# Performance work log

Hardware: AMD Instinct MI355X
Metric: run time of the kernel (lower is better)

## Reference

```python
import jax, jax.numpy as jnp
import numpy as np

T_STEPS = 32      # discrete samples along each pixel's voting ray
RAY_STEP = 4.0    # pixel stride between ray samples


def setup_inputs() -> dict:
    key = jax.random.key(0)
    k1, k2, k3, k4 = jax.random.split(key, 4)
    B, C, H, W = 2, 22, 480, 640
    label = jax.random.randint(k1, (B, H, W), 0, C, dtype=jnp.int32)
    vertex = jax.random.normal(k2, (B, 3 * C, H, W), dtype=jnp.float32)
    # per-class 3D extents in meters (~0..0.3 m objects)
    extents = jax.random.uniform(k3, (C, 3), dtype=jnp.float32) * 0.3
    # flattened intrinsics [fx, 0, cx, 0, fy, cy, 0, 0, 1]
    intr = jnp.array([572.4, 0.0, 325.3, 0.0, 573.6, 242.0, 0.0, 0.0, 1.0], dtype=jnp.float32)
    meta_data = jnp.tile(intr[None, :], (B, 1))
    gt = jax.random.normal(k4, (B, C, 4, 4), dtype=jnp.float32)
    return {"label": label, "vertex": vertex, "extents": extents,
            "meta_data": meta_data, "gt": gt, "is_train": 0}


def reference(label, vertex, extents, meta_data, gt, is_train):
    B, C3, H, W = vertex.shape
    C = C3 // 3
    HW = H * W
    f32 = jnp.float32

    # Gather each pixel's class-specific vertex prediction: (nx, ny, z)
    v = vertex.reshape(B, C, 3, HW)                        # (B,C,3,HW)
    lab = label.reshape(B, HW)                             # (B,HW) int
    idx = jnp.broadcast_to(lab[:, None, None, :], (B, 1, 3, HW))
    g = jnp.take_along_axis(v, idx, axis=1)[:, 0]          # (B,3,HW)
    nx, ny, z = g[:, 0], g[:, 1], g[:, 2]
    inv_norm = 1.0 / (jnp.sqrt(nx * nx + ny * ny) + 1e-8)
    nx = nx * inv_norm
    ny = ny * inv_norm

    # Pixel coordinates
    pix = jnp.arange(HW, dtype=jnp.int32)
    xs = (pix % W).astype(f32)
    ys = (pix // W).astype(f32)

    # Cast T_STEPS votes along the predicted ray toward the object center
    t = (jnp.arange(1, T_STEPS + 1, dtype=f32) * RAY_STEP)  # (T,)
    px = jnp.round(xs[None, :, None] + nx[:, :, None] * t[None, None, :]).astype(jnp.int32)
    py = jnp.round(ys[None, :, None] + ny[:, :, None] * t[None, None, :]).astype(jnp.int32)
    inb = (px >= 0) & (px < W) & (py >= 0) & (py < H)
    fg = (lab > 0)[:, :, None]                              # background casts no votes
    w = (inb & fg).astype(f32)                              # (B,HW,T)
    flat = jnp.clip(py, 0, H - 1) * W + jnp.clip(px, 0, W - 1)

    # Scatter-accumulate votes into per-class Hough space (B,C,HW)
    b_idx = jnp.arange(B)[:, None, None]
    acc = jnp.zeros((B, C, HW), dtype=f32).at[b_idx, lab[:, :, None], flat].add(w)

    # Peak detection: argmax per (batch, class)
    peak = jnp.argmax(acc, axis=-1)                         # (B,C)
    votes = jnp.max(acc, axis=-1)                           # (B,C)
    cx = (peak % W).astype(f32)
    cy = (peak // W).astype(f32)

    # Mean predicted depth per class (masked mean over that class's pixels)
    b2 = jnp.arange(B)[:, None]
    cnt = jnp.zeros((B, C), dtype=f32).at[b2, lab].add(1.0)
    zsum = jnp.zeros((B, C), dtype=f32).at[b2, lab].add(z)
    depth = zsum / jnp.maximum(cnt, 1.0)

    # Project object extents to image-plane box size: half = 0.5*|extent|*fx/depth
    fx = meta_data[:, 0][:, None]                           # (B,1)
    diag = jnp.linalg.norm(extents, axis=-1)[None, :]       # (1,C)
    half = 0.5 * diag * fx / jnp.maximum(jnp.abs(depth), 1e-3)

    cls = jnp.broadcast_to(jnp.arange(C, dtype=f32)[None, :], (B, C))
    out = jnp.stack([cls, votes,
                     cx - half, cy - half, cx + half, cy + half,
                     cx, cy, depth], axis=-1)               # (B,C,9)
    return out
```

## Files before the change

### kernel.cpp

```cpp
#include <hip/hip_runtime.h>


#define MAXC 32
#define NSEG 4

__global__ __launch_bounds__(512) void emit_kernel(
    const int* __restrict__ label, const float* __restrict__ vertex,
    unsigned short* __restrict__ bucketData, unsigned* __restrict__ cursor,
    unsigned* __restrict__ cnt, float* __restrict__ zsum,
    int C, int H, int W, int HW, int SEGCAP, int NB)
{
    __shared__ unsigned s_bin[512];
    __shared__ unsigned s_rel[512];
    __shared__ unsigned s_gb[512];
    __shared__ unsigned s_ccnt[MAXC];
    __shared__ float s_cz[MAXC];

    int tid = threadIdx.x;
    int b = blockIdx.y;
    int p = blockIdx.x * 512 + tid;
    int seg = blockIdx.x & (NSEG - 1);

    s_bin[tid] = 0u;
    s_rel[tid] = 0u;
    if (tid < MAXC) { s_ccnt[tid] = 0u; s_cz[tid] = 0.0f; }
    __syncthreads();

    int lab = 0;
    unsigned vote[32];
    bool fg = false;
    if (p < HW) {
        lab = label[(size_t)b * HW + p];
        const float* vb = vertex + ((size_t)(b * 3 * C + 3 * lab)) * HW + p;
        float nx = vb[0];
        float ny = vb[(size_t)HW];
        float z  = vb[2 * (size_t)HW];
        atomicAdd(&s_ccnt[lab], 1u);
        atomicAdd(&s_cz[lab], z);
        if (lab > 0) {
            fg = true;
            float nrm = __fsqrt_rn(__fadd_rn(__fmul_rn(nx, nx), __fmul_rn(ny, ny)));
            float inv = __fdiv_rn(1.0f, __fadd_rn(nrm, 1e-8f));
            float nxn = __fmul_rn(nx, inv);
            float nyn = __fmul_rn(ny, inv);
            float xs = (float)(p % W);
            float ys = (float)(p / W);
            #pragma unroll
            for (int i = 1; i <= 32; ++i) {
                float t = (float)i * 4.0f;
                int px = (int)rintf(__fadd_rn(xs, __fmul_rn(nxn, t)));
                int py = (int)rintf(__fadd_rn(ys, __fmul_rn(nyn, t)));
                vote[i - 1] = (px >= 0 && px < W && py >= 0 && py < H)
                            ? ((unsigned)(py << 10) | (unsigned)px) : 0xFFFFFFFFu;
            }
        }
    }
    if (!fg) {
        #pragma unroll
        for (int i = 0; i < 32; ++i) vote[i] = 0xFFFFFFFFu;
    }

    #pragma unroll
    for (int i = 0; i < 32; ++i)
        if (vote[i] != 0xFFFFFFFFu) atomicAdd(&s_bin[vote[i] >> 10], 1u);
    __syncthreads();

    if (tid < H) {
        unsigned n = s_bin[tid];
        s_gb[tid] = n ? atomicAdd(&cursor[seg * NB + b * H + tid], n) : 0u;
    }
    __syncthreads();

    unsigned labsh = (unsigned)lab << 10;
    #pragma unroll
    for (int i = 0; i < 32; ++i) {
        unsigned vt = vote[i];
        if (vt != 0xFFFFFFFFu) {
            unsigned py = vt >> 10;
            unsigned rel = atomicAdd(&s_rel[py], 1u);
            unsigned g = s_gb[py] + rel;
            if (g < (unsigned)SEGCAP)
                bucketData[((size_t)(b * H + py) * NSEG + seg) * SEGCAP + g] =
                    (unsigned short)(labsh | (vt & 1023u));
        }
    }

    if (tid < C) {
        unsigned c = s_ccnt[tid];
        if (c) {
            atomicAdd(&cnt[b * C + tid], c);
            atomicAdd(&zsum[b * C + tid], s_cz[tid]);
        }
    }
}

__global__ __launch_bounds__(256) void hist_kernel(
    const unsigned short* __restrict__ bucketData,
    const unsigned* __restrict__ cursor,
    unsigned long long* __restrict__ keys,
    int C, int H, int W, int SEGCAP, int NB)
{
    extern __shared__ char sm[];
    unsigned* hist = (unsigned*)sm;
    unsigned long long* s_wb =
        (unsigned long long*)(sm + (size_t)(C * W / 2) * 4);

    int tid = threadIdx.x;
    int lane = tid & 63, wave = tid >> 6;
    int py = blockIdx.x;
    int b = blockIdx.y;
    int words = C * W / 2;

    for (int i = tid; i < words; i += 256) hist[i] = 0u;
    __syncthreads();

    int bucket = b * H + py;
    #pragma unroll
    for (int seg = 0; seg < NSEG; ++seg) {
        unsigned n = cursor[seg * NB + bucket];
        if (n > (unsigned)SEGCAP) n = (unsigned)SEGCAP;
        const unsigned short* src =
            bucketData + ((size_t)bucket * NSEG + seg) * SEGCAP;
        for (unsigned i = tid; i < n; i += 256) {
            unsigned r = src[i];
            unsigned idx = (r >> 10) * (unsigned)W + (r & 1023u);
            atomicAdd(&hist[idx >> 1], 1u << ((idx & 1u) * 16));
        }
    }
    __syncthreads();

    unsigned rowbase = (unsigned)py * (unsigned)W;
    for (int c = 0; c < C; ++c) {
        unsigned long long best = 0;
        for (int px = tid; px < W; px += 256) {
            unsigned cv = (hist[(unsigned)(c * W + px) >> 1] >> ((px & 1) * 16)) & 0xFFFFu;
            unsigned long long k = ((unsigned long long)cv << 32)
                                 | (unsigned long long)(0xFFFFFFFFu - (rowbase + px));
            if (k > best) best = k;
        }
        #pragma unroll
        for (int off = 32; off > 0; off >>= 1) {
            unsigned long long o = __shfl_xor(best, off, 64);
            if (o > best) best = o;
        }
        if (lane == 0) s_wb[c * 4 + wave] = best;
    }
    __syncthreads();
    if (tid < C) {
        unsigned long long m = s_wb[tid * 4];
        #pragma unroll
        for (int w2 = 1; w2 < 4; ++w2)
            if (s_wb[tid * 4 + w2] > m) m = s_wb[tid * 4 + w2];
        atomicMax(&keys[b * C + tid], m);
    }
}

__global__ void finalize_kernel(const unsigned long long* __restrict__ keys,
                                const unsigned* __restrict__ cnt,
                                const float* __restrict__ zsum,
                                const float* __restrict__ extents,
                                const float* __restrict__ meta,
                                float* __restrict__ out,
                                int B, int C, int W)
{
    int i = threadIdx.x;
    if (i >= B * C) return;
    int b = i / C, c = i % C;
    unsigned long long k = keys[i];
    unsigned votes = (unsigned)(k >> 32);
    unsigned peak = 0xFFFFFFFFu - (unsigned)(k & 0xFFFFFFFFull);
    float cx = (float)(peak % (unsigned)W);
    float cy = (float)(peak / (unsigned)W);
    float n = (float)cnt[i];
    float depth = zsum[i] / fmaxf(n, 1.0f);
    float fx = meta[b * 9 + 0];
    const float* e = extents + c * 3;
    float diag = sqrtf(e[0] * e[0] + e[1] * e[1] + e[2] * e[2]);
    float half = 0.5f * diag * fx / fmaxf(fabsf(depth), 0.001f);
    float* o = out + (size_t)i * 9;
    o[0] = (float)c;
    o[1] = (float)votes;
    o[2] = cx - half;
    o[3] = cy - half;
    o[4] = cx + half;
    o[5] = cy + half;
    o[6] = cx;
    o[7] = cy;
    o[8] = depth;
}

extern "C" void kernel_launch(void* const* d_in, const int* in_sizes, int n_in,
                              void* d_out, int out_size, void* d_ws, size_t ws_size,
                              hipStream_t stream)
{
    const int* label    = (const int*)d_in[0];
    const float* vertex = (const float*)d_in[1];
    const float* extents= (const float*)d_in[2];
    const float* meta   = (const float*)d_in[3];

    int C = in_sizes[2] / 3;
    int B = in_sizes[3] / 9;
    int HW = in_sizes[0] / B;
    const int W = 640;
    int H = HW / W;
    int NB = B * H;

    size_t keysOff = 0;
    size_t curOff  = keysOff + (size_t)B * C * 8;
    size_t cntOff  = curOff + (size_t)NSEG * NB * 4;
    size_t zsumOff = cntOff + (size_t)B * C * 4;
    size_t zeroEnd = zsumOff + (size_t)B * C * 4;
    size_t dataOff = (zeroEnd + 63) & ~(size_t)63;

    size_t availRec = (ws_size > dataOff) ? (ws_size - dataOff) / ((size_t)NB * NSEG * 2) : 0;
    int SEGCAP = (int)(availRec > 8192 ? 8192 : availRec);
    SEGCAP &= ~63;

    unsigned long long* keys = (unsigned long long*)((char*)d_ws + keysOff);
    unsigned* cursor         = (unsigned*)((char*)d_ws + curOff);
    unsigned* cnt            = (unsigned*)((char*)d_ws + cntOff);
    float* zsum              = (float*)((char*)d_ws + zsumOff);
    unsigned short* bucketData = (unsigned short*)((char*)d_ws + dataOff);

    hipMemsetAsync(d_ws, 0, zeroEnd, stream);

    dim3 egrid((HW + 511) / 512, B);
    emit_kernel<<<egrid, 512, 0, stream>>>(label, vertex, bucketData, cursor,
                                           cnt, zsum, C, H, W, HW, SEGCAP, NB);

    dim3 hgrid(H, B);
    size_t hsm = (size_t)(C * W / 2) * 4 + (size_t)C * 4 * 8;
    hist_kernel<<<hgrid, 256, hsm, stream>>>(bucketData, cursor, keys, C, H, W, SEGCAP, NB);

    finalize_kernel<<<1, 64, 0, stream>>>(keys, cnt, zsum, extents, meta,
                                          (float*)d_out, B, C, W);
}
```

Measured before the change: 121.7 us.

## Split emit kernel into count and scatter passes that recompute ray votes

Splits the single emit kernel into two launches. The first computes ray samples and builds per-block row counts, then reserves global bucket space and stores the per-block offsets in a workspace table. The second recomputes the same ray samples and scatters records using those offsets. This removes the 32-entry per-thread vote array held across barriers, aiming to cut register pressure and raise occupancy. In exchange the label and vertex data are read twice, the ray arithmetic is done twice, and there is an extra launch plus a global offset table.

```diff
diff --git a/kernel.cpp b/kernel.cpp
--- a/kernel.cpp
+++ b/kernel.cpp
@@ -4,15 +4,37 @@
 #define MAXC 32
 #define NSEG 4
 
-__global__ __launch_bounds__(512) void emit_kernel(
+__device__ __forceinline__ void ray_setup(
     const int* __restrict__ label, const float* __restrict__ vertex,
-    unsigned short* __restrict__ bucketData, unsigned* __restrict__ cursor,
+    int C, int HW, int W, int b, int p,
+    int& lab, float& z, bool& fg,
+    float& nxn, float& nyn, float& xs, float& ys)
+{
+    lab = label[(size_t)b * HW + p];
+    const float* vb = vertex + ((size_t)(b * 3 * C + 3 * lab)) * HW + p;
+    float nx = vb[0];
+    float ny = vb[(size_t)HW];
+    z = vb[2 * (size_t)HW];
+    fg = false;
+    nxn = 0.f; nyn = 0.f; xs = 0.f; ys = 0.f;
+    if (lab > 0) {
+        fg = true;
+        float nrm = __fsqrt_rn(__fadd_rn(__fmul_rn(nx, nx), __fmul_rn(ny, ny)));
+        float inv = __fdiv_rn(1.0f, __fadd_rn(nrm, 1e-8f));
+        nxn = __fmul_rn(nx, inv);
+        nyn = __fmul_rn(ny, inv);
+        xs = (float)(p % W);
+        ys = (float)(p / W);
+    }
+}
+
+__global__ __launch_bounds__(512) void emitA_kernel(
+    const int* __restrict__ label, const float* __restrict__ vertex,
+    unsigned* __restrict__ cursor, unsigned* __restrict__ gbTable,
     unsigned* __restrict__ cnt, float* __restrict__ zsum,
-    int C, int H, int W, int HW, int SEGCAP, int NB)
+    int C, int H, int W, int HW, int NB)
 {
     __shared__ unsigned s_bin[512];
-    __shared__ unsigned s_rel[512];
-    __shared__ unsigned s_gb[512];
     __shared__ unsigned s_ccnt[MAXC];
     __shared__ float s_cz[MAXC];
 
@@ -22,67 +44,31 @@
     int seg = blockIdx.x & (NSEG - 1);
 
     s_bin[tid] = 0u;
-    s_rel[tid] = 0u;
     if (tid < MAXC) { s_ccnt[tid] = 0u; s_cz[tid] = 0.0f; }
     __syncthreads();
 
-    int lab = 0;
-    unsigned vote[32];
-    bool fg = false;
     if (p < HW) {
-        lab = label[(size_t)b * HW + p];
-        const float* vb = vertex + ((size_t)(b * 3 * C + 3 * lab)) * HW + p;
-        float nx = vb[0];
-        float ny = vb[(size_t)HW];
-        float z  = vb[2 * (size_t)HW];
+        int lab; float z; bool fg; float nxn, nyn, xs, ys;
+        ray_setup(label, vertex, C, HW, W, b, p, lab, z, fg, nxn, nyn, xs, ys);
         atomicAdd(&s_ccnt[lab], 1u);
         atomicAdd(&s_cz[lab], z);
-        if (lab > 0) {
-            fg = true;
-            float nrm = __fsqrt_rn(__fadd_rn(__fmul_rn(nx, nx), __fmul_rn(ny, ny)));
-            float inv = __fdiv_rn(1.0f, __fadd_rn(nrm, 1e-8f));
-            float nxn = __fmul_rn(nx, inv);
-            float nyn = __fmul_rn(ny, inv);
-            float xs = (float)(p % W);
-            float ys = (float)(p / W);
+        if (fg) {
             #pragma unroll
             for (int i = 1; i <= 32; ++i) {
                 float t = (float)i * 4.0f;
                 int px = (int)rintf(__fadd_rn(xs, __fmul_rn(nxn, t)));
                 int py = (int)rintf(__fadd_rn(ys, __fmul_rn(nyn, t)));
-                vote[i - 1] = (px >= 0 && px < W && py >= 0 && py < H)
-                            ? ((unsigned)(py << 10) | (unsigned)px) : 0xFFFFFFFFu;
+                if (px >= 0 && px < W && py >= 0 && py < H)
+                    atomicAdd(&s_bin[py], 1u);
             }
         }
     }
-    if (!fg) {
-        #pragma unroll
-        for (int i = 0; i < 32; ++i) vote[i] = 0xFFFFFFFFu;
-    }
-
-    #pragma unroll
-    for (int i = 0; i < 32; ++i)
-        if (vote[i] != 0xFFFFFFFFu) atomicAdd(&s_bin[vote[i] >> 10], 1u);
     __syncthreads();
 
     if (tid < H) {
         unsigned n = s_bin[tid];
-        s_gb[tid] = n ? atomicAdd(&cursor[seg * NB + b * H + tid], n) : 0u;
-    }
-    __syncthreads();
-
-    unsigned labsh = (unsigned)lab << 10;
-    #pragma unroll
-    for (int i = 0; i < 32; ++i) {
-        unsigned vt = vote[i];
-        if (vt != 0xFFFFFFFFu) {
-            unsigned py = vt >> 10;
-            unsigned rel = atomicAdd(&s_rel[py], 1u);
-            unsigned g = s_gb[py] + rel;
-            if (g < (unsigned)SEGCAP)
-                bucketData[((size_t)(b * H + py) * NSEG + seg) * SEGCAP + g] =
-                    (unsigned short)(labsh | (vt & 1023u));
-        }
+        unsigned base = n ? atomicAdd(&cursor[seg * NB + b * H + tid], n) : 0u;
+        gbTable[(size_t)(b * gridDim.x + blockIdx.x) * 512 + tid] = base;
     }
 
     if (tid < C) {
@@ -90,6 +76,45 @@
         if (c) {
             atomicAdd(&cnt[b * C + tid], c);
             atomicAdd(&zsum[b * C + tid], s_cz[tid]);
+        }
+    }
+}
+
+__global__ __launch_bounds__(512) void emitB_kernel(
+    const int* __restrict__ label, const float* __restrict__ vertex,
+    const unsigned* __restrict__ gbTable, unsigned short* __restrict__ bucketData,
+    int C, int H, int W, int HW, int SEGCAP, int NB)
+{
+    __shared__ unsigned s_rel[512];
+    __shared__ unsigned s_gb[512];
+
+    int tid = threadIdx.x;
+    int b = blockIdx.y;
+    int p = blockIdx.x * 512 + tid;
+    int seg = blockIdx.x & (NSEG - 1);
+
+    s_rel[tid] = 0u;
+    s_gb[tid] = gbTable[(size_t)(b * gridDim.x + blockIdx.x) * 512 + tid];
+    __syncthreads();
+
+    if (p < HW) {
+        int lab; float z; bool fg; float nxn, nyn, xs, ys;
+        ray_setup(label, vertex, C, HW, W, b, p, lab, z, fg, nxn, nyn, xs, ys);
+        if (fg) {
+            unsigned labsh = (unsigned)lab << 10;
+            #pragma unroll
+            for (int i = 1; i <= 32; ++i) {
+                float t = (float)i * 4.0f;
+                int px = (int)rintf(__fadd_rn(xs, __fmul_rn(nxn, t)));
+                int py = (int)rintf(__fadd_rn(ys, __fmul_rn(nyn, t)));
+                if (px >= 0 && px < W && py >= 0 && py < H) {
+                    unsigned rel = atomicAdd(&s_rel[py], 1u);
+                    unsigned g = s_gb[py] + rel;
+                    if (g < (unsigned)SEGCAP)
+                        bucketData[((size_t)(b * H + py) * NSEG + seg) * SEGCAP + g] =
+                            (unsigned short)(labsh | (unsigned)px);
+                }
+            }
         }
     }
 }
@@ -204,13 +229,16 @@
     const int W = 640;
     int H = HW / W;
     int NB = B * H;
+    int GX = (HW + 511) / 512;
 
     size_t keysOff = 0;
     size_t curOff  = keysOff + (size_t)B * C * 8;
     size_t cntOff  = curOff + (size_t)NSEG * NB * 4;
     size_t zsumOff = cntOff + (size_t)B * C * 4;
     size_t zeroEnd = zsumOff + (size_t)B * C * 4;
-    size_t dataOff = (zeroEnd + 63) & ~(size_t)63;
+    size_t gbOff   = (zeroEnd + 63) & ~(size_t)63;
+    size_t gbBytes = (size_t)B * GX * 512 * 4;
+    size_t dataOff = (gbOff + gbBytes + 63) & ~(size_t)63;
 
     size_t availRec = (ws_size > dataOff) ? (ws_size - dataOff) / ((size_t)NB * NSEG * 2) : 0;
     int SEGCAP = (int)(availRec > 8192 ? 8192 : availRec);
@@ -220,13 +248,16 @@
     unsigned* cursor         = (unsigned*)((char*)d_ws + curOff);
     unsigned* cnt            = (unsigned*)((char*)d_ws + cntOff);
     float* zsum              = (float*)((char*)d_ws + zsumOff);
+    unsigned* gbTable        = (unsigned*)((char*)d_ws + gbOff);
     unsigned short* bucketData = (unsigned short*)((char*)d_ws + dataOff);
 
     hipMemsetAsync(d_ws, 0, zeroEnd, stream);
 
-    dim3 egrid((HW + 511) / 512, B);
-    emit_kernel<<<egrid, 512, 0, stream>>>(label, vertex, bucketData, cursor,
-                                           cnt, zsum, C, H, W, HW, SEGCAP, NB);
+    dim3 egrid(GX, B);
+    emitA_kernel<<<egrid, 512, 0, stream>>>(label, vertex, cursor, gbTable,
+                                            cnt, zsum, C, H, W, HW, NB);
+    emitB_kernel<<<egrid, 512, 0, stream>>>(label, vertex, gbTable, bucketData,
+                                            C, H, W, HW, SEGCAP, NB);
 
     dim3 hgrid(H, B);
     size_t hsm = (size_t)(C * W / 2) * 4 + (size_t)C * 4 * 8;
```

Measured after the change: 144.9 us. 19.1% more time.
